# Kernel tuning notes

Hardware: AMD Instinct MI355X
Metric: run time of the kernel (lower is better)

The kernel has to match this reference:

```python
import jax, jax.numpy as jnp
import numpy as np

B, N, H = 1024, 128, 128
T = 2 * N  # max_steps default: 2 * n_nodes
NEG = -1e9
TEMPERATURE = 1.0


def setup_inputs() -> dict:
    key = jax.random.key(0)
    ks = jax.random.split(key, 12)
    coords = jax.random.uniform(ks[0], (B, N, 2), dtype=jnp.float32)
    demands = jax.random.uniform(ks[1], (B, N), dtype=jnp.float32) * 0.3
    demands = demands.at[:, 0].set(0.0)  # depot has zero demand
    capacities = jnp.ones((B,), jnp.float32)
    s = 0.1
    return dict(
        coords=coords, demands=demands, capacities=capacities,
        W_emb=jax.random.normal(ks[2], (3, H), jnp.float32) * s, b_emb=jnp.zeros((H,), jnp.float32),
        Wq=jax.random.normal(ks[3], (H, H), jnp.float32) * s, bq=jnp.zeros((H,), jnp.float32),
        Wk=jax.random.normal(ks[4], (H, H), jnp.float32) * s, bk=jnp.zeros((H,), jnp.float32),
        Wv=jax.random.normal(ks[5], (H, H), jnp.float32) * s, bv=jnp.zeros((H,), jnp.float32),
        Wp1=jax.random.normal(ks[6], (2 * H, H), jnp.float32) * s, bp1=jnp.zeros((H,), jnp.float32),
        Wp2=jax.random.normal(ks[7], (H, 1), jnp.float32) * s, bp2=jnp.zeros((1,), jnp.float32),
    )


def _forward(coords, demands, capacities, W_emb, b_emb, Wq, bq, Wk, bk, Wv, bv, Wp1, bp1, Wp2, bp2):
    # --- encoder: single self-attention pass (done once, outside the decode loop) ---
    nf = jnp.concatenate([coords, demands[..., None]], axis=-1)           # [B,N,3]
    emb = nf @ W_emb + b_emb                                               # [B,N,H]
    Q = emb @ Wq + bq
    K = emb @ Wk + bk
    V = emb @ Wv + bv
    attn = jax.nn.softmax(jnp.einsum('bnh,bmh->bnm', Q, K) / jnp.sqrt(jnp.float32(H)), axis=-1)
    att_emb = jnp.einsum('bnm,bmh->bnh', attn, V)                          # [B,N,H]
    idx = jnp.arange(N)

    def step(carry, key_t):
        visited, rem_cap, at_depot, done = carry
        # done when all customers visited and currently at depot
        done = done | (visited[:, 1:].all(-1) & at_depot)
        # context = masked mean of unvisited node embeddings (zeros if none)
        unvis = (~visited).astype(att_emb.dtype)                           # [B,N]
        cnt = unvis.sum(-1, keepdims=True)
        ctx = jnp.einsum('bn,bnh->bh', unvis, att_emb) / jnp.maximum(cnt, 1.0)
        pin = jnp.concatenate([att_emb, jnp.broadcast_to(ctx[:, None, :], att_emb.shape)], -1)
        sc = (jax.nn.relu(pin @ Wp1 + bp1) @ Wp2 + bp2)[..., 0]            # [B,N]
        # feasibility mask: visited, over-capacity, depot-if-at-depot
        mask = visited | (demands > rem_cap[:, None])
        mask = mask.at[:, 0].set(mask[:, 0] | at_depot)
        all_masked = mask.all(-1)
        # if everything masked and not at depot -> allow returning to depot
        mask = mask.at[:, 0].set(mask[:, 0] & ~(all_masked & ~at_depot))
        # if everything masked and at depot -> done
        done = done | (all_masked & at_depot)
        # keep logits finite for done rows (their log-prob is zeroed below)
        mask = mask.at[:, 0].set(mask[:, 0] & ~done)
        logits = jnp.where(mask, NEG, sc) / TEMPERATURE
        lp = jax.nn.log_softmax(logits, axis=-1)
        action = jax.random.categorical(key_t, logits)                     # multinomial sampling
        sel = jnp.take_along_axis(lp, action[:, None], 1)[:, 0]
        sel = jnp.where(done, 0.0, sel)
        action = jnp.where(done, 0, action)
        is_depot = action == 0
        upd = ~done
        visited = visited | ((idx[None, :] == action[:, None]) & (upd & ~is_depot)[:, None])
        d_taken = jnp.take_along_axis(demands, action[:, None], 1)[:, 0]
        rem_cap = jnp.where(upd, jnp.where(is_depot, capacities, rem_cap - d_taken), rem_cap)
        at_depot = jnp.where(upd, is_depot, at_depot)
        return (visited, rem_cap, at_depot, done), (action, sel)

    keys = jax.random.split(jax.random.key(42), T)
    init = (jnp.zeros((B, N), bool), capacities, jnp.ones((B,), bool), jnp.zeros((B,), bool))
    _, (actions, lps) = jax.lax.scan(step, init, keys)
    return actions.T, lps.sum(0)  # routes [B,T] (0-padded when done), combined log-probs [B]


def reference(coords, demands, capacities, W_emb, b_emb, Wq, bq, Wk, bk, Wv, bv, Wp1, bp1, Wp2, bp2):
    return _forward(coords, demands, capacities, W_emb, b_emb, Wq, bq, Wk, bk, Wv, bv, Wp1, bp1, Wp2, bp2)
```

## Files before the change

kernel.cpp:

```cpp
#include <hip/hip_runtime.h>
#include <stdint.h>
#include <stddef.h>


#define NEGV (-1e9f)

__device__ __forceinline__ uint32_t rotl32(uint32_t v, int d) { return (v << d) | (v >> (32 - d)); }

__device__ __forceinline__ void threefry2x32(uint32_t k0, uint32_t k1, uint32_t c0, uint32_t c1,
                                             uint32_t& o0, uint32_t& o1) {
  uint32_t k2 = k0 ^ k1 ^ 0x1BD11BDAu;
  uint32_t x0 = c0 + k0, x1 = c1 + k1;
  x0 += x1; x1 = rotl32(x1, 13); x1 ^= x0;
  x0 += x1; x1 = rotl32(x1, 15); x1 ^= x0;
  x0 += x1; x1 = rotl32(x1, 26); x1 ^= x0;
  x0 += x1; x1 = rotl32(x1, 6);  x1 ^= x0;
  x0 += k1; x1 += k2 + 1u;
  x0 += x1; x1 = rotl32(x1, 17); x1 ^= x0;
  x0 += x1; x1 = rotl32(x1, 29); x1 ^= x0;
  x0 += x1; x1 = rotl32(x1, 16); x1 ^= x0;
  x0 += x1; x1 = rotl32(x1, 24); x1 ^= x0;
  x0 += k2; x1 += k0 + 2u;
  x0 += x1; x1 = rotl32(x1, 13); x1 ^= x0;
  x0 += x1; x1 = rotl32(x1, 15); x1 ^= x0;
  x0 += x1; x1 = rotl32(x1, 26); x1 ^= x0;
  x0 += x1; x1 = rotl32(x1, 6);  x1 ^= x0;
  x0 += k0; x1 += k1 + 3u;
  x0 += x1; x1 = rotl32(x1, 17); x1 ^= x0;
  x0 += x1; x1 = rotl32(x1, 29); x1 ^= x0;
  x0 += x1; x1 = rotl32(x1, 16); x1 ^= x0;
  x0 += x1; x1 = rotl32(x1, 24); x1 ^= x0;
  x0 += k1; x1 += k2 + 4u;
  x0 += x1; x1 = rotl32(x1, 13); x1 ^= x0;
  x0 += x1; x1 = rotl32(x1, 15); x1 ^= x0;
  x0 += x1; x1 = rotl32(x1, 26); x1 ^= x0;
  x0 += x1; x1 = rotl32(x1, 6);  x1 ^= x0;
  x0 += k2; x1 += k0 + 5u;
  o0 = x0; o1 = x1;
}

__device__ __forceinline__ float gumbel_from(uint32_t kA, uint32_t kB, uint32_t idx) {
  uint32_t o0, o1;
  threefry2x32(kA, kB, 0u, idx, o0, o1);
  uint32_t bits = o0 ^ o1;
  uint32_t mb = bits >> 9;
  float u = (mb == 0u) ? 1.17549435e-38f : (float)mb * 1.1920928955078125e-07f;
  return -logf(-logf(u));
}

__device__ void mm128(const float* Alds, float* wst,
                      const float* __restrict__ W, const float* __restrict__ bias,
                      float* outg, int t) {
  int wv = t >> 6, lane = t & 63;
  int j0 = lane * 2;
  float b0 = 0.f, b1 = 0.f;
  if (bias) { b0 = bias[j0]; b1 = bias[j0 + 1]; }
  int r0 = wv * 32;
  float acc0[4][8], acc1[4][8];
#pragma unroll
  for (int g = 0; g < 4; ++g)
#pragma unroll
    for (int r = 0; r < 8; ++r) { acc0[g][r] = b0; acc1[g][r] = b1; }
  for (int ks = 0; ks < 128; ks += 16) {
    __syncthreads();
    for (int i = t; i < 2048; i += 256) wst[i] = W[ks * 128 + i];
    __syncthreads();
#pragma unroll
    for (int k4 = 0; k4 < 16; k4 += 4) {
      float2 w[4];
#pragma unroll
      for (int kk = 0; kk < 4; ++kk) w[kk] = *(const float2*)&wst[(k4 + kk) * 128 + j0];
#pragma unroll
      for (int g = 0; g < 4; ++g)
#pragma unroll
        for (int r = 0; r < 8; ++r) {
          float4 a = *(const float4*)&Alds[(r0 + g * 8 + r) * 128 + ks + k4];
          acc0[g][r] = fmaf(a.x, w[0].x, acc0[g][r]); acc1[g][r] = fmaf(a.x, w[0].y, acc1[g][r]);
          acc0[g][r] = fmaf(a.y, w[1].x, acc0[g][r]); acc1[g][r] = fmaf(a.y, w[1].y, acc1[g][r]);
          acc0[g][r] = fmaf(a.z, w[2].x, acc0[g][r]); acc1[g][r] = fmaf(a.z, w[2].y, acc1[g][r]);
          acc0[g][r] = fmaf(a.w, w[3].x, acc0[g][r]); acc1[g][r] = fmaf(a.w, w[3].y, acc1[g][r]);
        }
    }
  }
#pragma unroll
  for (int g = 0; g < 4; ++g)
#pragma unroll
    for (int r = 0; r < 8; ++r) {
      int n = r0 + g * 8 + r;
      float2 o; o.x = acc0[g][r]; o.y = acc1[g][r];
      *(float2*)&outg[n * 128 + j0] = o;
    }
}

__global__ __launch_bounds__(256, 2) void pn_e1(
    const float* __restrict__ coords, const float* __restrict__ demands,
    const float* __restrict__ W_emb, const float* __restrict__ b_emb,
    const float* __restrict__ Wq, const float* __restrict__ bq,
    const float* __restrict__ Wk, const float* __restrict__ bk,
    const float* __restrict__ Wv, const float* __restrict__ bv,
    float* Qo, float* Ko, float* Vo) {
  __shared__ float emb[128 * 128];
  __shared__ float wst[16 * 128];
  __shared__ float nfx[128], nfy[128], nfd[128];
  int b = blockIdx.x, t = threadIdx.x;
  if (t < 128) {
    float2 c = ((const float2*)coords)[b * 128 + t];
    nfx[t] = c.x; nfy[t] = c.y; nfd[t] = demands[b * 128 + t];
  }
  __syncthreads();
  {
    int h = t >> 1, n0 = (t & 1) * 64;
    float w0 = W_emb[h], w1 = W_emb[128 + h], w2 = W_emb[256 + h], be = b_emb[h];
    for (int n = n0; n < n0 + 64; ++n) {
      float e = nfx[n] * w0;
      e = fmaf(nfy[n], w1, e);
      e = fmaf(nfd[n], w2, e);
      e = e + be;
      emb[n * 128 + h] = e;
    }
  }
  __syncthreads();
  mm128(emb, wst, Wq, bq, Qo + (size_t)b * 16384, t);
  mm128(emb, wst, Wk, bk, Ko + (size_t)b * 16384, t);
  mm128(emb, wst, Wv, bv, Vo + (size_t)b * 16384, t);
}

__global__ __launch_bounds__(256, 2) void pn_e2(
    const float* Qg, const float* __restrict__ Kg, const float* __restrict__ Vg, float* atto) {
  __shared__ float Ks[128 * 132];
  __shared__ float qb[4 * 512];
  int b = blockIdx.x, t = threadIdx.x;
  int wv = t >> 6, lane = t & 63;
  const float sden = sqrtf(128.0f);
  for (int i = t; i < 16384; i += 256) {
    int m = i >> 7, k = i & 127;
    Ks[m * 132 + k] = Kg[(size_t)b * 16384 + i];
  }
  __syncthreads();
  const float* Vb = Vg + (size_t)b * 16384;
  for (int pass = 0; pass < 8; ++pass) {
    int nb = pass * 16 + wv * 4;
    for (int i = lane; i < 512; i += 64) qb[wv * 512 + i] = Qg[(size_t)b * 16384 + nb * 128 + i];
    __syncthreads();
    float s0[4] = {0.f, 0.f, 0.f, 0.f}, s1[4] = {0.f, 0.f, 0.f, 0.f};
    for (int k = 0; k < 128; k += 4) {
      float4 ka = *(const float4*)&Ks[lane * 132 + k];
      float4 kb = *(const float4*)&Ks[(lane + 64) * 132 + k];
#pragma unroll
      for (int r = 0; r < 4; ++r) {
        float4 q = *(const float4*)&qb[wv * 512 + r * 128 + k];
        s0[r] = fmaf(q.x, ka.x, s0[r]); s0[r] = fmaf(q.y, ka.y, s0[r]);
        s0[r] = fmaf(q.z, ka.z, s0[r]); s0[r] = fmaf(q.w, ka.w, s0[r]);
        s1[r] = fmaf(q.x, kb.x, s1[r]); s1[r] = fmaf(q.y, kb.y, s1[r]);
        s1[r] = fmaf(q.z, kb.z, s1[r]); s1[r] = fmaf(q.w, kb.w, s1[r]);
      }
    }
    float p0[4], p1[4];
#pragma unroll
    for (int r = 0; r < 4; ++r) {
      float a0 = s0[r] / sden, a1 = s1[r] / sden;
      float mx = fmaxf(a0, a1);
#pragma unroll
      for (int off = 1; off < 64; off <<= 1) mx = fmaxf(mx, __shfl_xor(mx, off));
      float e0 = expf(a0 - mx), e1 = expf(a1 - mx);
      float sm = e0 + e1;
#pragma unroll
      for (int off = 1; off < 64; off <<= 1) sm += __shfl_xor(sm, off);
      p0[r] = e0 / sm; p1[r] = e1 / sm;
    }
#pragma unroll
    for (int r = 0; r < 4; ++r) {
      qb[wv * 512 + r * 128 + lane] = p0[r];
      qb[wv * 512 + r * 128 + lane + 64] = p1[r];
    }
    __syncthreads();
    float o0[4] = {0.f, 0.f, 0.f, 0.f}, o1[4] = {0.f, 0.f, 0.f, 0.f};
    for (int m4 = 0; m4 < 128; m4 += 4) {
      float4 p[4];
#pragma unroll
      for (int r = 0; r < 4; ++r) p[r] = *(const float4*)&qb[wv * 512 + r * 128 + m4];
#pragma unroll
      for (int mm = 0; mm < 4; ++mm) {
        float v0 = Vb[(m4 + mm) * 128 + lane];
        float v1 = Vb[(m4 + mm) * 128 + lane + 64];
#pragma unroll
        for (int r = 0; r < 4; ++r) {
          float pv = (mm == 0) ? p[r].x : (mm == 1) ? p[r].y : (mm == 2) ? p[r].z : p[r].w;
          o0[r] = fmaf(pv, v0, o0[r]);
          o1[r] = fmaf(pv, v1, o1[r]);
        }
      }
    }
#pragma unroll
    for (int r = 0; r < 4; ++r) {
      atto[(size_t)b * 16384 + (nb + r) * 128 + lane] = o0[r];
      atto[(size_t)b * 16384 + (nb + r) * 128 + lane + 64] = o1[r];
    }
    __syncthreads();
  }
}

__global__ __launch_bounds__(256, 2) void pn_e3(
    const float* attg, const float* __restrict__ Wp1,
    const float* __restrict__ bp1, float* A1o, float* Po) {
  __shared__ float att[128 * 128];
  __shared__ float wst[16 * 128];
  int b = blockIdx.x, t = threadIdx.x;
  for (int i = t; i < 16384; i += 256) att[i] = attg[(size_t)b * 16384 + i];
  __syncthreads();
  mm128(att, wst, Wp1, bp1, A1o + (size_t)b * 16384, t);
  mm128(att, wst, Wp1 + 16384, (const float*)0, Po + (size_t)b * 16384, t);
}

__global__ __launch_bounds__(256, 2) void pn_decode(
    const float* __restrict__ A1g, const float* __restrict__ Pg,
    const float* __restrict__ demands, const float* __restrict__ caps,
    const float* __restrict__ Wp2, const float* __restrict__ bp2, float* out) {
  __shared__ __align__(16) float P[128 * 128];
  __shared__ __align__(16) float c1[128];
  __shared__ float scv[128];
  __shared__ float dem[128];
  __shared__ float gv[3][128];
  __shared__ int acts[256];
  __shared__ uint32_t keyA[256], keyB[256];
  __shared__ int doneFlag;

  int b = blockIdx.x, t = threadIdx.x;
  int wave = t >> 6, lane = t & 63;
  { uint32_t o0, o1; threefry2x32(0u, 42u, 0u, (uint32_t)t, o0, o1); keyA[t] = o0; keyB[t] = o1; }
  for (int i = t; i < 16384; i += 256) P[i] = Pg[(size_t)b * 16384 + i];
  int nrow = t >> 1, half = t & 1;
  float a1r[64], w2r[64];
  {
    const float4* asrc = (const float4*)(A1g + (size_t)b * 16384 + nrow * 128 + half * 64);
    const float4* wsrc = (const float4*)(Wp2 + half * 64);
#pragma unroll
    for (int j = 0; j < 16; ++j) {
      float4 v = asrc[j];
      a1r[4 * j] = v.x; a1r[4 * j + 1] = v.y; a1r[4 * j + 2] = v.z; a1r[4 * j + 3] = v.w;
      float4 w = wsrc[j];
      w2r[4 * j] = w.x; w2r[4 * j + 1] = w.y; w2r[4 * j + 2] = w.z; w2r[4 * j + 3] = w.w;
    }
  }
  if (t < 128) dem[t] = demands[b * 128 + t];
  acts[t] = 0;
  if (t == 0) doneFlag = 0;
  float capv = caps[b];
  float bp2v = bp2[0];
  float dem0 = 0.f, dem1 = 0.f;
  if (wave < 2) {
    dem0 = demands[b * 128 + lane];
    dem1 = demands[b * 128 + lane + 64];
  }
  unsigned long long vism0 = 0ull, vism1 = 0ull;
  float rc = capv, lps = 0.f;
  int at = 1, done = 0, vc = 0;
  __syncthreads();
  if (t >= 128) gv[0][t - 128] = gumbel_from(keyA[0], keyB[0], (uint32_t)(b * 128 + (t - 128)));

  int rslot = 0;
  for (int step = 0; step < 256; ++step) {
    int wslot = rslot + 1; if (wslot == 3) wslot = 0;
    if (t < 128) {
      uint32_t m0 = __builtin_amdgcn_readfirstlane((uint32_t)(vism0 & 0xffffffffull));
      uint32_t m1 = __builtin_amdgcn_readfirstlane((uint32_t)(vism0 >> 32));
      uint32_t m2 = __builtin_amdgcn_readfirstlane((uint32_t)(vism1 & 0xffffffffull));
      uint32_t m3 = __builtin_amdgcn_readfirstlane((uint32_t)(vism1 >> 32));
      float cnt = fmaxf((float)(128 - vc), 1.f);
      const float* pc = &P[t];
      float acc = 0.f;
#pragma unroll
      for (int n = 0; n < 128; n += 2) {
        float pa = pc[n * 128];
        float pb = pc[(n + 1) * 128];
        uint32_t wa = (n < 32) ? m0 : (n < 64) ? m1 : (n < 96) ? m2 : m3;
        uint32_t wb = ((n + 1) < 32) ? m0 : ((n + 1) < 64) ? m1 : ((n + 1) < 96) ? m2 : m3;
        float sa = ((wa >> (n & 31)) & 1u) ? 0.f : 1.f;
        float sb = ((wb >> ((n + 1) & 31)) & 1u) ? 0.f : 1.f;
        acc = fmaf(pa, sa, acc);
        acc = fmaf(pb, sb, acc);
      }
      c1[t] = acc / cnt;
    } else if (step < 255) {
      int n = t - 128;
      gv[wslot][n] = gumbel_from(keyA[step + 1], keyB[step + 1], (uint32_t)(b * 128 + n));
    }
    __syncthreads();
    if (doneFlag) break;

    {
      const float* crow = &c1[half * 64];
      float acc = 0.f;
#pragma unroll
      for (int q = 0; q < 16; ++q) {
        float4 c4 = *(const float4*)&crow[q * 4];
        float x;
        x = a1r[4 * q] + c4.x;     x = fmaxf(x, 0.f); acc = fmaf(x, w2r[4 * q], acc);
        x = a1r[4 * q + 1] + c4.y; x = fmaxf(x, 0.f); acc = fmaf(x, w2r[4 * q + 1], acc);
        x = a1r[4 * q + 2] + c4.z; x = fmaxf(x, 0.f); acc = fmaf(x, w2r[4 * q + 2], acc);
        x = a1r[4 * q + 3] + c4.w; x = fmaxf(x, 0.f); acc = fmaf(x, w2r[4 * q + 3], acc);
      }
      float other = __shfl_xor(acc, 1);
      if (half == 0) scv[nrow] = (acc + other) + bp2v;
    }
    __syncthreads();

    if (t < 128) {
      float g0 = gv[rslot][lane], g1 = gv[rslot][lane + 64];
      bool mk0 = (lane == 0) ? (at != 0)
                             : ((((vism0 >> lane) & 1ull) != 0ull) || (dem0 > rc));
      bool mk1 = (((vism1 >> lane) & 1ull) != 0ull) || (dem1 > rc);
      unsigned long long bl0 = __ballot(mk0 ? 1 : 0);
      unsigned long long bl1 = __ballot(mk1 ? 1 : 0);
      int d = done;
      if (vc == 127 && at) d = 1;
      if ((bl0 == ~0ull) && (bl1 == ~0ull) && at) d = 1;
      if (lane == 0) mk0 = (at && !d);
      float sc0 = scv[lane], sc1 = scv[lane + 64];
      float lg0 = mk0 ? NEGV : sc0;
      float lg1 = mk1 ? NEGV : sc1;
      float v0g = g0 + lg0, v1g = g1 + lg1;
      float v; int idx;
      if (v1g > v0g) { v = v1g; idx = lane + 64; } else { v = v0g; idx = lane; }
      float mx = fmaxf(lg0, lg1);
#pragma unroll
      for (int off = 1; off < 64; off <<= 1) {
        float ov = __shfl_xor(v, off);
        int oi = __shfl_xor(idx, off);
        if (ov > v || (ov == v && oi < idx)) { v = ov; idx = oi; }
        mx = fmaxf(mx, __shfl_xor(mx, off));
      }
      int a = d ? 0 : idx;
      if (wave == 0) {
        float e = expf(lg0 - mx) + expf(lg1 - mx);
#pragma unroll
        for (int off = 1; off < 64; off <<= 1) e += __shfl_xor(e, off);
        if (lane == 0) {
          float sel = d ? 0.f : ((scv[idx] - mx) - logf(e));
          lps += sel;
          acts[step] = a;
          doneFlag = d;
        }
      }
      if (!d) {
        if (a == 0) { rc = capv; at = 1; }
        else {
          rc = rc - dem[a];
          at = 0; vc = vc + 1;
          if (a < 64) vism0 |= (1ull << a); else vism1 |= (1ull << (a - 64));
        }
      }
      done = d;
    }
    rslot = wslot;
  }

  __syncthreads();
  out[(size_t)b * 256 + t] = (float)acts[t];
  if (t == 0) out[(size_t)1024 * 256 + b] = lps;
}

extern "C" void kernel_launch(void* const* d_in, const int* in_sizes, int n_in,
                              void* d_out, int out_size, void* d_ws, size_t ws_size,
                              hipStream_t stream) {
  (void)in_sizes; (void)n_in; (void)out_size; (void)ws_size;
  const float* coords  = (const float*)d_in[0];
  const float* demands = (const float*)d_in[1];
  const float* caps    = (const float*)d_in[2];
  const float* W_emb   = (const float*)d_in[3];
  const float* b_emb   = (const float*)d_in[4];
  const float* Wq      = (const float*)d_in[5];
  const float* bq      = (const float*)d_in[6];
  const float* Wk      = (const float*)d_in[7];
  const float* bk      = (const float*)d_in[8];
  const float* Wv      = (const float*)d_in[9];
  const float* bv      = (const float*)d_in[10];
  const float* Wp1     = (const float*)d_in[11];
  const float* bp1     = (const float*)d_in[12];
  const float* Wp2     = (const float*)d_in[13];
  const float* bp2     = (const float*)d_in[14];

  float* ws = (float*)d_ws;
  const size_t R = (size_t)1024 * 128 * 128;
  float* R0 = ws;
  float* R1 = ws + R;
  float* R2 = ws + 2 * R;

  pn_e1<<<1024, 256, 0, stream>>>(coords, demands, W_emb, b_emb, Wq, bq, Wk, bk, Wv, bv, R0, R1, R2);
  pn_e2<<<1024, 256, 0, stream>>>(R0, R1, R2, R0);
  pn_e3<<<1024, 256, 0, stream>>>(R0, Wp1, bp1, R0, R1);
  pn_decode<<<1024, 256, 0, stream>>>(R0, R1, demands, caps, Wp2, bp2, (float*)d_out);
}
```

Before: 2.301 ms.

## Keep P columns in registers and drop the 64KB shared P tile

Removes the 64KB shared-memory copy of P, so threads 128-255 each hold one P column in registers and compute the context vector there. Threads 0-127 now hold two A1 rows each and compute scores for two nodes, reading Wp2 from shared memory, while all waves run the selection logic redundantly. This is meant to cut LDS traffic and LDS footprint, allowing more blocks per CU and avoiding strided shared reads. The cost is a 128-float register array per thread, which may spill or lower occupancy, and half the threads now do the score work that all threads shared before.

```diff
diff --git a/kernel.cpp b/kernel.cpp
--- a/kernel.cpp
+++ b/kernel.cpp
@@ -216,8 +216,8 @@
     const float* __restrict__ A1g, const float* __restrict__ Pg,
     const float* __restrict__ demands, const float* __restrict__ caps,
     const float* __restrict__ Wp2, const float* __restrict__ bp2, float* out) {
-  __shared__ __align__(16) float P[128 * 128];
   __shared__ __align__(16) float c1[128];
+  __shared__ __align__(16) float wp2s[128];
   __shared__ float scv[128];
   __shared__ float dem[128];
   __shared__ float gv[3][128];
@@ -228,84 +228,89 @@
   int b = blockIdx.x, t = threadIdx.x;
   int wave = t >> 6, lane = t & 63;
   { uint32_t o0, o1; threefry2x32(0u, 42u, 0u, (uint32_t)t, o0, o1); keyA[t] = o0; keyB[t] = o1; }
-  for (int i = t; i < 16384; i += 256) P[i] = Pg[(size_t)b * 16384 + i];
-  int nrow = t >> 1, half = t & 1;
-  float a1r[64], w2r[64];
-  {
-    const float4* asrc = (const float4*)(A1g + (size_t)b * 16384 + nrow * 128 + half * 64);
-    const float4* wsrc = (const float4*)(Wp2 + half * 64);
-#pragma unroll
-    for (int j = 0; j < 16; ++j) {
-      float4 v = asrc[j];
-      a1r[4 * j] = v.x; a1r[4 * j + 1] = v.y; a1r[4 * j + 2] = v.z; a1r[4 * j + 3] = v.w;
-      float4 w = wsrc[j];
-      w2r[4 * j] = w.x; w2r[4 * j + 1] = w.y; w2r[4 * j + 2] = w.z; w2r[4 * j + 3] = w.w;
-    }
-  }
-  if (t < 128) dem[t] = demands[b * 128 + t];
+  if (t < 128) { dem[t] = demands[b * 128 + t]; wp2s[t] = Wp2[t]; }
   acts[t] = 0;
   if (t == 0) doneFlag = 0;
+
+  int nrow = t >> 1, half = t & 1;
+  float rf[128];
+  if (t < 128) {
+    const float4* asrc0 = (const float4*)(A1g + (size_t)b * 16384 + nrow * 128 + half * 64);
+    const float4* asrc1 = (const float4*)(A1g + (size_t)b * 16384 + (nrow + 64) * 128 + half * 64);
+#pragma unroll
+    for (int j = 0; j < 16; ++j) {
+      float4 v = asrc0[j];
+      rf[4 * j] = v.x; rf[4 * j + 1] = v.y; rf[4 * j + 2] = v.z; rf[4 * j + 3] = v.w;
+      float4 w = asrc1[j];
+      rf[64 + 4 * j] = w.x; rf[64 + 4 * j + 1] = w.y; rf[64 + 4 * j + 2] = w.z; rf[64 + 4 * j + 3] = w.w;
+    }
+  } else {
+    int h = t - 128;
+    const float* pc = Pg + (size_t)b * 16384 + h;
+#pragma unroll
+    for (int n = 0; n < 128; ++n) rf[n] = pc[n * 128];
+  }
   float capv = caps[b];
   float bp2v = bp2[0];
-  float dem0 = 0.f, dem1 = 0.f;
-  if (wave < 2) {
-    dem0 = demands[b * 128 + lane];
-    dem1 = demands[b * 128 + lane + 64];
-  }
+  float dem0 = demands[b * 128 + lane];
+  float dem1 = demands[b * 128 + lane + 64];
   unsigned long long vism0 = 0ull, vism1 = 0ull;
   float rc = capv, lps = 0.f;
   int at = 1, done = 0, vc = 0;
   __syncthreads();
-  if (t >= 128) gv[0][t - 128] = gumbel_from(keyA[0], keyB[0], (uint32_t)(b * 128 + (t - 128)));
+  if (t < 128) gv[0][t] = gumbel_from(keyA[0], keyB[0], (uint32_t)(b * 128 + t));
 
   int rslot = 0;
   for (int step = 0; step < 256; ++step) {
     int wslot = rslot + 1; if (wslot == 3) wslot = 0;
-    if (t < 128) {
+    if (t >= 128) {
       uint32_t m0 = __builtin_amdgcn_readfirstlane((uint32_t)(vism0 & 0xffffffffull));
       uint32_t m1 = __builtin_amdgcn_readfirstlane((uint32_t)(vism0 >> 32));
       uint32_t m2 = __builtin_amdgcn_readfirstlane((uint32_t)(vism1 & 0xffffffffull));
       uint32_t m3 = __builtin_amdgcn_readfirstlane((uint32_t)(vism1 >> 32));
       float cnt = fmaxf((float)(128 - vc), 1.f);
-      const float* pc = &P[t];
       float acc = 0.f;
 #pragma unroll
-      for (int n = 0; n < 128; n += 2) {
-        float pa = pc[n * 128];
-        float pb = pc[(n + 1) * 128];
-        uint32_t wa = (n < 32) ? m0 : (n < 64) ? m1 : (n < 96) ? m2 : m3;
-        uint32_t wb = ((n + 1) < 32) ? m0 : ((n + 1) < 64) ? m1 : ((n + 1) < 96) ? m2 : m3;
-        float sa = ((wa >> (n & 31)) & 1u) ? 0.f : 1.f;
-        float sb = ((wb >> ((n + 1) & 31)) & 1u) ? 0.f : 1.f;
-        acc = fmaf(pa, sa, acc);
-        acc = fmaf(pb, sb, acc);
-      }
-      c1[t] = acc / cnt;
+      for (int n = 0; n < 128; ++n) {
+        uint32_t mw = (n < 32) ? m0 : (n < 64) ? m1 : (n < 96) ? m2 : m3;
+        float s = ((mw >> (n & 31)) & 1u) ? 0.f : 1.f;
+        acc = fmaf(rf[n], s, acc);
+      }
+      c1[t - 128] = acc / cnt;
     } else if (step < 255) {
-      int n = t - 128;
-      gv[wslot][n] = gumbel_from(keyA[step + 1], keyB[step + 1], (uint32_t)(b * 128 + n));
+      gv[wslot][t] = gumbel_from(keyA[step + 1], keyB[step + 1], (uint32_t)(b * 128 + t));
     }
     __syncthreads();
     if (doneFlag) break;
 
-    {
+    if (t < 128) {
       const float* crow = &c1[half * 64];
-      float acc = 0.f;
+      const float* wrow = &wp2s[half * 64];
+      float acca = 0.f, accb = 0.f;
 #pragma unroll
       for (int q = 0; q < 16; ++q) {
         float4 c4 = *(const float4*)&crow[q * 4];
+        float4 w4 = *(const float4*)&wrow[q * 4];
         float x;
-        x = a1r[4 * q] + c4.x;     x = fmaxf(x, 0.f); acc = fmaf(x, w2r[4 * q], acc);
-        x = a1r[4 * q + 1] + c4.y; x = fmaxf(x, 0.f); acc = fmaf(x, w2r[4 * q + 1], acc);
-        x = a1r[4 * q + 2] + c4.z; x = fmaxf(x, 0.f); acc = fmaf(x, w2r[4 * q + 2], acc);
-        x = a1r[4 * q + 3] + c4.w; x = fmaxf(x, 0.f); acc = fmaf(x, w2r[4 * q + 3], acc);
-      }
-      float other = __shfl_xor(acc, 1);
-      if (half == 0) scv[nrow] = (acc + other) + bp2v;
-    }
-    __syncthreads();
-
-    if (t < 128) {
+        x = rf[4 * q] + c4.x;          x = fmaxf(x, 0.f); acca = fmaf(x, w4.x, acca);
+        x = rf[4 * q + 1] + c4.y;      x = fmaxf(x, 0.f); acca = fmaf(x, w4.y, acca);
+        x = rf[4 * q + 2] + c4.z;      x = fmaxf(x, 0.f); acca = fmaf(x, w4.z, acca);
+        x = rf[4 * q + 3] + c4.w;      x = fmaxf(x, 0.f); acca = fmaf(x, w4.w, acca);
+        x = rf[64 + 4 * q] + c4.x;     x = fmaxf(x, 0.f); accb = fmaf(x, w4.x, accb);
+        x = rf[64 + 4 * q + 1] + c4.y; x = fmaxf(x, 0.f); accb = fmaf(x, w4.y, accb);
+        x = rf[64 + 4 * q + 2] + c4.z; x = fmaxf(x, 0.f); accb = fmaf(x, w4.z, accb);
+        x = rf[64 + 4 * q + 3] + c4.w; x = fmaxf(x, 0.f); accb = fmaf(x, w4.w, accb);
+      }
+      float oa = __shfl_xor(acca, 1);
+      float ob = __shfl_xor(accb, 1);
+      if (half == 0) {
+        scv[nrow] = (acca + oa) + bp2v;
+        scv[nrow + 64] = (accb + ob) + bp2v;
+      }
+    }
+    __syncthreads();
+
+    {
       float g0 = gv[rslot][lane], g1 = gv[rslot][lane + 64];
       bool mk0 = (lane == 0) ? (at != 0)
                              : ((((vism0 >> lane) & 1ull) != 0ull) || (dem0 > rc));
```

Result: faster. 2.142 ms (-6.9%).
